# Kernel optimization log

Hardware: AMD Instinct MI355X
Metric: run time of the kernel (lower is better)

## Reference

```python
import jax, jax.numpy as jnp
import numpy as np

N1 = 50000        # nodes in g1
N_LAYERS = 3
N2 = N1 * N_LAYERS  # nodes in g2 (kron tiling)
E1 = 800000
E2 = 2400000
D = 64
LEAKY_SLOPE = 0.01


def graph_conv(x, src, dst, num_nodes, W, b):
    """DGL GraphConv with norm='both', in_feats == out_feats (aggregate-then-matmul).
    h = D_in^{-1/2} A D_out^{-1/2} x W + b, degrees clamped to >=1.
    """
    ones_e = jnp.ones(src.shape[0], dtype=x.dtype)
    out_deg = jax.ops.segment_sum(ones_e, src, num_segments=num_nodes)
    in_deg = jax.ops.segment_sum(ones_e, dst, num_segments=num_nodes)
    norm_src = jnp.power(jnp.clip(out_deg, 1.0), -0.5)  # [N]
    norm_dst = jnp.power(jnp.clip(in_deg, 1.0), -0.5)   # [N]
    feat = x * norm_src[:, None]                         # [N, D]
    agg = jax.ops.segment_sum(feat[src], dst, num_segments=num_nodes)  # [N, D]
    rst = agg * norm_dst[:, None]
    return rst @ W + b


def setup_inputs() -> dict:
    key = jax.random.key(0)
    k = jax.random.split(key, 8)
    return {
        "node_features": jax.random.normal(k[0], (N1, D), dtype=jnp.float32),
        "WQ": jax.random.normal(k[1], (D, D), dtype=jnp.float32) * (1.0 / np.sqrt(D)),
        "bQ": jnp.zeros((D,), dtype=jnp.float32),
        "WM": jax.random.normal(k[2], (D, D), dtype=jnp.float32) * (1.0 / np.sqrt(D)),
        "bM": jnp.zeros((D,), dtype=jnp.float32),
        "src1": jax.random.randint(k[3], (E1,), 0, N1, dtype=jnp.int32),
        "dst1": jax.random.randint(k[4], (E1,), 0, N1, dtype=jnp.int32),
        "src2": jax.random.randint(k[5], (E2,), 0, N2, dtype=jnp.int32),
        "dst2": jax.random.randint(k[6], (E2,), 0, N2, dtype=jnp.int32),
    }


def reference(node_features, WQ, bQ, WM, bM, src1, dst1, src2, dst2):
    h_Q1 = graph_conv(node_features, src1, dst1, N1, WQ, bQ)
    h_Q1 = jax.nn.leaky_relu(h_Q1, negative_slope=LEAKY_SLOPE)
    # torch.kron(ones(n_layers,1), h_Q1) == vertical tiling
    M_feat = jnp.tile(h_Q1, (N_LAYERS, 1))  # [N_LAYERS*N1, D]
    h_M1 = graph_conv(M_feat, src2, dst2, N2, WM, bM)
    return jax.nn.leaky_relu(h_M1, negative_slope=LEAKY_SLOPE)
```

## Files before the change

kernel.cpp:

```cpp
#include <hip/hip_runtime.h>
#include <hip/hip_fp16.h>

constexpr int cN1 = 50000;
constexpr int cN2 = 150000;
constexpr int cE1 = 800000;
constexpr int cE2 = 2400000;
constexpr int cD  = 64;
constexpr int MAXB = 640;
#define LEAKY 0.01f

constexpr int NB1 = (cN1 + 255) / 256;
constexpr int NB2 = (cN2 + 255) / 256;

constexpr int BD1 = 64, BD2 = 192, BS1 = 64, BS2 = 192, CVB = 256;
constexpr int PR0 = BD1;
constexpr int PR1 = PR0 + BD2;
constexpr int PR2 = PR1 + BS1;
constexpr int PR3 = PR2 + BS2;
constexpr int PR4 = PR3 + CVB;

constexpr int SD1 = 128, SD2 = 384, SS1 = 64, SS2 = 192;

__device__ __forceinline__ void bucket_count_region(
    const int* __restrict__ idx, int E4, int* __restrict__ bcnt, int nbuck,
    int b, int B, int* h) {
    for (int i = threadIdx.x; i < nbuck; i += 256) h[i] = 0;
    __syncthreads();
    const int4* v4 = (const int4*)idx;
    for (int i = b * 256 + threadIdx.x; i < E4; i += B * 256) {
        int4 v = v4[i];
        atomicAdd(&h[v.x >> 8], 1);
        atomicAdd(&h[v.y >> 8], 1);
        atomicAdd(&h[v.z >> 8], 1);
        atomicAdd(&h[v.w >> 8], 1);
    }
    __syncthreads();
    for (int i = threadIdx.x; i < nbuck; i += 256) {
        int c = h[i];
        if (c) atomicAdd(&bcnt[i], c);
    }
}

__global__ __launch_bounds__(256) void prep_kernel(
    const int* __restrict__ dst1, const int* __restrict__ dst2,
    const int* __restrict__ src1, const int* __restrict__ src2,
    const float* __restrict__ x, __half* __restrict__ xh,
    int* __restrict__ bcntD1, int* __restrict__ bcntD2,
    int* __restrict__ bcntS1, int* __restrict__ bcntS2) {
    __shared__ int h[MAXB];
    int b = blockIdx.x;
    if (b < PR0) {
        bucket_count_region(dst1, cE1 / 4, bcntD1, NB1, b, BD1, h);
    } else if (b < PR1) {
        bucket_count_region(dst2, cE2 / 4, bcntD2, NB2, b - PR0, BD2, h);
    } else if (b < PR2) {
        bucket_count_region(src1, cE1 / 4, bcntS1, NB1, b - PR1, BS1, h);
    } else if (b < PR3) {
        bucket_count_region(src2, cE2 / 4, bcntS2, NB2, b - PR2, BS2, h);
    } else {
        int i = (b - PR3) * 256 + threadIdx.x;
        const int n4 = cN1 * cD / 4;
        for (; i < n4; i += CVB * 256) {
            float4 v = ((const float4*)x)[i];
            __half2* o = (__half2*)xh;
            o[2 * i]     = __floats2half2_rn(v.x, v.y);
            o[2 * i + 1] = __floats2half2_rn(v.z, v.w);
        }
    }
}

__global__ __launch_bounds__(256) void scan4_kernel(
    int* __restrict__ bcntD1, int* __restrict__ bbaseD1, int* __restrict__ bcurD1,
    int* __restrict__ bcntD2, int* __restrict__ bbaseD2, int* __restrict__ bcurD2,
    int* __restrict__ bcntS1, int* __restrict__ bbaseS1, int* __restrict__ bcurS1,
    int* __restrict__ bcntS2, int* __restrict__ bbaseS2, int* __restrict__ bcurS2,
    int* __restrict__ offs1, int* __restrict__ offs2) {
    int b = blockIdx.x;
    int tid = threadIdx.x;
    int* bcnt; int* bbase; int* bcur; int n; int e;
    if (b == 0)      { bcnt = bcntD1; bbase = bbaseD1; bcur = bcurD1; n = NB1; e = cE1; }
    else if (b == 1) { bcnt = bcntD2; bbase = bbaseD2; bcur = bcurD2; n = NB2; e = cE2; }
    else if (b == 2) { bcnt = bcntS1; bbase = bbaseS1; bcur = bcurS1; n = NB1; e = cE1; }
    else             { bcnt = bcntS2; bbase = bbaseS2; bcur = bcurS2; n = NB2; e = cE2; }
    if (b == 0 && tid == 0) offs1[cN1] = cE1;
    if (b == 1 && tid == 0) offs2[cN2] = cE2;
    __shared__ int s[256];
    int v[4];
    int t = 0;
#pragma unroll
    for (int j = 0; j < 4; ++j) { int i = tid * 4 + j; v[j] = (i < n) ? bcnt[i] : 0; t += v[j]; }
    s[tid] = t; __syncthreads();
    for (int off = 1; off < 256; off <<= 1) {
        int a = (tid >= off) ? s[tid - off] : 0;
        __syncthreads();
        s[tid] += a;
        __syncthreads();
    }
    int run = s[tid] - t;
#pragma unroll
    for (int j = 0; j < 4; ++j) {
        int i = tid * 4 + j;
        if (i < n) { bbase[i] = run; bcur[i] = run; run += v[j]; }
    }
    if (tid == 0) bbase[n] = e;
}

__global__ __launch_bounds__(256) void scatter4_kernel(
    const int* __restrict__ src1, const int* __restrict__ dst1,
    int* __restrict__ bcurD1, unsigned int* __restrict__ pairs1,
    const int* __restrict__ src2, const int* __restrict__ dst2,
    int* __restrict__ bcurD2, unsigned int* __restrict__ pairs2,
    int* __restrict__ bcurS1, unsigned char* __restrict__ sval1,
    int* __restrict__ bcurS2, unsigned char* __restrict__ sval2) {
    __shared__ int hist[MAXB];
    __shared__ int cur[MAXB];
    int tid = threadIdx.x;
    int bx = blockIdx.x;
    bool pairMode;
    const int* key; const int* pay; int* bcur;
    unsigned int* pout = nullptr; unsigned char* bout = nullptr;
    int nbuck, E, blk, nblk;
    if (bx < SD1) {
        pairMode = true;  key = dst1; pay = src1; bcur = bcurD1; pout = pairs1;
        nbuck = NB1; E = cE1; blk = bx; nblk = SD1;
    } else if (bx < SD1 + SD2) {
        pairMode = true;  key = dst2; pay = src2; bcur = bcurD2; pout = pairs2;
        nbuck = NB2; E = cE2; blk = bx - SD1; nblk = SD2;
    } else if (bx < SD1 + SD2 + SS1) {
        pairMode = false; key = src1; pay = nullptr; bcur = bcurS1; bout = sval1;
        nbuck = NB1; E = cE1; blk = bx - SD1 - SD2; nblk = SS1;
    } else {
        pairMode = false; key = src2; pay = nullptr; bcur = bcurS2; bout = sval2;
        nbuck = NB2; E = cE2; blk = bx - SD1 - SD2 - SS1; nblk = SS2;
    }
    int spe = (((E / 4) + nblk - 1) / nblk) * 4;
    int b0 = blk * spe;
    int b1 = b0 + spe; if (b1 > E) b1 = E;
    for (int i = tid; i < nbuck; i += 256) hist[i] = 0;
    __syncthreads();
    for (int i = b0 + tid * 4; i < b1; i += 1024) {
        int4 d = *(const int4*)(key + i);
        atomicAdd(&hist[d.x >> 8], 1);
        atomicAdd(&hist[d.y >> 8], 1);
        atomicAdd(&hist[d.z >> 8], 1);
        atomicAdd(&hist[d.w >> 8], 1);
    }
    __syncthreads();
    for (int i = tid; i < nbuck; i += 256) cur[i] = atomicAdd(&bcur[i], hist[i]);
    __syncthreads();
    if (pairMode) {
        for (int i = b0 + tid * 4; i < b1; i += 1024) {
            int4 d = *(const int4*)(key + i);
            int4 s = *(const int4*)(pay + i);
            int p0 = atomicAdd(&cur[d.x >> 8], 1);
            pout[p0] = ((unsigned)(d.x & 255) << 24) | (unsigned)s.x;
            int p1 = atomicAdd(&cur[d.y >> 8], 1);
            pout[p1] = ((unsigned)(d.y & 255) << 24) | (unsigned)s.y;
            int p2 = atomicAdd(&cur[d.z >> 8], 1);
            pout[p2] = ((unsigned)(d.z & 255) << 24) | (unsigned)s.z;
            int p3 = atomicAdd(&cur[d.w >> 8], 1);
            pout[p3] = ((unsigned)(d.w & 255) << 24) | (unsigned)s.w;
        }
    } else {
        for (int i = b0 + tid * 4; i < b1; i += 1024) {
            int4 d = *(const int4*)(key + i);
            int p0 = atomicAdd(&cur[d.x >> 8], 1); bout[p0] = (unsigned char)(d.x & 255);
            int p1 = atomicAdd(&cur[d.y >> 8], 1); bout[p1] = (unsigned char)(d.y & 255);
            int p2 = atomicAdd(&cur[d.z >> 8], 1); bout[p2] = (unsigned char)(d.z & 255);
            int p3 = atomicAdd(&cur[d.w >> 8], 1); bout[p3] = (unsigned char)(d.w & 255);
        }
    }
}

__global__ __launch_bounds__(256) void sbin_kernel(
    const unsigned char* __restrict__ sval1, const int* __restrict__ bbaseS1,
    float* __restrict__ nsrc1,
    const unsigned char* __restrict__ sval2, const int* __restrict__ bbaseS2,
    float* __restrict__ nsrc2) {
    const unsigned char* sv; const int* bbase; float* nsrc; int N, bk;
    if (blockIdx.x < NB1) { sv = sval1; bbase = bbaseS1; nsrc = nsrc1; N = cN1; bk = blockIdx.x; }
    else                  { sv = sval2; bbase = bbaseS2; nsrc = nsrc2; N = cN2; bk = blockIdx.x - NB1; }
    __shared__ int cnt[256];
    int tid = threadIdx.x;
    cnt[tid] = 0;
    __syncthreads();
    int k0 = bbase[bk];
    int k1 = bbase[bk + 1];
    for (int k = k0 + tid; k < k1; k += 256) atomicAdd(&cnt[sv[k]], 1);
    __syncthreads();
    int lo = bk << 8;
    int span = N - lo; if (span > 256) span = 256;
    if (tid < span) {
        int d = cnt[tid];
        d = d < 1 ? 1 : d;
        nsrc[lo + tid] = rsqrtf((float)d);
    }
}

__global__ __launch_bounds__(256) void bin12_kernel(
    const unsigned int* __restrict__ pairs1, const int* __restrict__ bbase1,
    const float* __restrict__ nsrc1, unsigned int* __restrict__ sorted1,
    int* __restrict__ offs1,
    const unsigned int* __restrict__ pairs2, const int* __restrict__ bbase2,
    const float* __restrict__ nsrc2, unsigned int* __restrict__ sorted2,
    int* __restrict__ offs2) {
    const unsigned int* pairs; const int* bbase; const float* nsrc;
    unsigned int* sorted; int* offs; int N, foldn, bk;
    if (blockIdx.x < NB1) {
        pairs = pairs1; bbase = bbase1; nsrc = nsrc1; sorted = sorted1;
        offs = offs1; N = cN1; foldn = 0; bk = blockIdx.x;
    } else {
        pairs = pairs2; bbase = bbase2; nsrc = nsrc2; sorted = sorted2;
        offs = offs2; N = cN2; foldn = cN1; bk = blockIdx.x - NB1;
    }
    __shared__ int cnt[256];
    __shared__ int s[256];
    __shared__ int cur[256];
    int tid = threadIdx.x;
    int lo = bk << 8;
    int span = N - lo; if (span > 256) span = 256;
    int k0 = bbase[bk];
    int k1 = bbase[bk + 1];
    cnt[tid] = 0;
    __syncthreads();
    for (int k = k0 + tid; k < k1; k += 256) atomicAdd(&cnt[pairs[k] >> 24], 1);
    __syncthreads();
    int v = cnt[tid];
    s[tid] = v; __syncthreads();
    for (int off = 1; off < 256; off <<= 1) {
        int a = (tid >= off) ? s[tid - off] : 0;
        __syncthreads();
        s[tid] += a;
        __syncthreads();
    }
    int excl = s[tid] - v;
    cur[tid] = k0 + excl;
    if (tid < span) offs[lo + tid] = k0 + excl;
    __syncthreads();
    for (int k = k0 + tid; k < k1; k += 256) {
        unsigned pr = pairs[k];
        int d = pr >> 24;
        int sidx = (int)(pr & 0xFFFFFFu);
        int r = sidx;
        if (foldn) {
            if (r >= 2 * foldn) r -= 2 * foldn;
            else if (r >= foldn) r -= foldn;
        }
        __half nh = __float2half(nsrc[sidx]);
        int pos = atomicAdd(&cur[d], 1);
        sorted[pos] = ((unsigned)__half_as_ushort(nh) << 16) | (unsigned)r;
    }
}

#define FMA8(v, nv)                                                     \
    {                                                                   \
        float2 f0 = __half22float2(*(const __half2*)&(v).x);            \
        float2 f1 = __half22float2(*(const __half2*)&(v).y);            \
        float2 f2 = __half22float2(*(const __half2*)&(v).z);            \
        float2 f3 = __half22float2(*(const __half2*)&(v).w);            \
        a0.x = fmaf(f0.x, nv, a0.x); a0.y = fmaf(f0.y, nv, a0.y);       \
        a0.z = fmaf(f1.x, nv, a0.z); a0.w = fmaf(f1.y, nv, a0.w);       \
        a1.x = fmaf(f2.x, nv, a1.x); a1.y = fmaf(f2.y, nv, a1.y);       \
        a1.z = fmaf(f3.x, nv, a1.z); a1.w = fmaf(f3.y, nv, a1.w);       \
    }

template <bool EPI>
__global__ __launch_bounds__(256) void agg_csr_kernel(
    const __half* __restrict__ feat, const unsigned int* __restrict__ sorted,
    const int* __restrict__ offs, float* __restrict__ outp,
    const float* __restrict__ bias, int N) {
    int w = (blockIdx.x * blockDim.x + threadIdx.x) >> 4;
    if (w >= N) return;
    int l16  = threadIdx.x & 15;
    int slot = l16 >> 3;
    int c    = l16 & 7;

    int k0 = offs[w];
    int k1 = offs[w + 1];
    float4 a0 = {0.f, 0.f, 0.f, 0.f};
    float4 a1 = {0.f, 0.f, 0.f, 0.f};

    int k = k0 + slot;
    for (; k + 2 < k1; k += 4) {
        unsigned eA = sorted[k];
        unsigned eB = sorted[k + 2];
        float nA = __half2float(__ushort_as_half((unsigned short)(eA >> 16)));
        float nB = __half2float(__ushort_as_half((unsigned short)(eB >> 16)));
        int rA = (int)(eA & 0xFFFFu);
        int rB = (int)(eB & 0xFFFFu);
        uint4 vA = *(const uint4*)(feat + (size_t)rA * cD + c * 8);
        uint4 vB = *(const uint4*)(feat + (size_t)rB * cD + c * 8);
        FMA8(vA, nA);
        FMA8(vB, nB);
    }
    if (k < k1) {
        unsigned e = sorted[k];
        float nv = __half2float(__ushort_as_half((unsigned short)(e >> 16)));
        int r = (int)(e & 0xFFFFu);
        uint4 v = *(const uint4*)(feat + (size_t)r * cD + c * 8);
        FMA8(v, nv);
    }

    a0.x += __shfl_xor(a0.x, 8); a0.y += __shfl_xor(a0.y, 8);
    a0.z += __shfl_xor(a0.z, 8); a0.w += __shfl_xor(a0.w, 8);
    a1.x += __shfl_xor(a1.x, 8); a1.y += __shfl_xor(a1.y, 8);
    a1.z += __shfl_xor(a1.z, 8); a1.w += __shfl_xor(a1.w, 8);

    if (slot == 0) {
        if (EPI) {
            int dg = k1 - k0;
            float nd = rsqrtf((float)(dg < 1 ? 1 : dg));
            float4 b0 = *(const float4*)(bias + c * 8);
            float4 b1 = *(const float4*)(bias + c * 8 + 4);
            float4 r0, r1;
            r0.x = fmaf(a0.x, nd, b0.x); r0.y = fmaf(a0.y, nd, b0.y);
            r0.z = fmaf(a0.z, nd, b0.z); r0.w = fmaf(a0.w, nd, b0.w);
            r1.x = fmaf(a1.x, nd, b1.x); r1.y = fmaf(a1.y, nd, b1.y);
            r1.z = fmaf(a1.z, nd, b1.z); r1.w = fmaf(a1.w, nd, b1.w);
            r0.x = r0.x > 0.f ? r0.x : LEAKY * r0.x;
            r0.y = r0.y > 0.f ? r0.y : LEAKY * r0.y;
            r0.z = r0.z > 0.f ? r0.z : LEAKY * r0.z;
            r0.w = r0.w > 0.f ? r0.w : LEAKY * r0.w;
            r1.x = r1.x > 0.f ? r1.x : LEAKY * r1.x;
            r1.y = r1.y > 0.f ? r1.y : LEAKY * r1.y;
            r1.z = r1.z > 0.f ? r1.z : LEAKY * r1.z;
            r1.w = r1.w > 0.f ? r1.w : LEAKY * r1.w;
            *(float4*)(outp + (size_t)w * cD + c * 8) = r0;
            *(float4*)(outp + (size_t)w * cD + c * 8 + 4) = r1;
        } else {
            *(float4*)(outp + (size_t)w * cD + c * 8) = a0;
            *(float4*)(outp + (size_t)w * cD + c * 8 + 4) = a1;
        }
    }
}
#undef FMA8

constexpr int GR = 32;
constexpr int RP = 36;

__global__ __launch_bounds__(256) void gemm12_kernel(
    const float* __restrict__ A, const int* __restrict__ offs,
    const float* __restrict__ WQ_, const float* __restrict__ bQ_,
    const float* __restrict__ WM_, __half* __restrict__ g, int N) {
    __shared__ float W1s[64 * 64];
    __shared__ float W2s[64 * 64];
    __shared__ float Rs_t[64 * RP];
    __shared__ float Hs_t[64 * RP];
    __shared__ float rn_s[GR];
    int tid = threadIdx.x;
    int row0 = blockIdx.x * GR;

    for (int i = tid; i < 64 * 64; i += 256) {
        W1s[i] = WQ_[i];
        W2s[i] = WM_[i];
    }
    if (tid < GR) {
        int row = row0 + tid;
        if (row < N) {
            int dg = offs[row + 1] - offs[row];
            rn_s[tid] = rsqrtf((float)(dg < 1 ? 1 : dg));
        } else {
            rn_s[tid] = 0.f;
        }
    }
    __syncthreads();
    for (int i = tid; i < GR * 64; i += 256) {
        int r = i >> 6;
        int k = i & 63;
        int row = row0 + r;
        float v = (row < N) ? A[(size_t)row * cD + k] * rn_s[r] : 0.f;
        Rs_t[k * RP + r] = v;
    }
    __syncthreads();

    int j  = tid & 63;
    int gq = tid >> 6;
    int r0 = gq * 8;

    float acc[8];
    float bq = bQ_[j];
#pragma unroll
    for (int i = 0; i < 8; ++i) acc[i] = bq;
#pragma unroll 8
    for (int k = 0; k < 64; ++k) {
        float wv = W1s[k * 64 + j];
        float4 ra = *(const float4*)&Rs_t[k * RP + r0];
        float4 rb = *(const float4*)&Rs_t[k * RP + r0 + 4];
        acc[0] = fmaf(ra.x, wv, acc[0]); acc[1] = fmaf(ra.y, wv, acc[1]);
        acc[2] = fmaf(ra.z, wv, acc[2]); acc[3] = fmaf(ra.w, wv, acc[3]);
        acc[4] = fmaf(rb.x, wv, acc[4]); acc[5] = fmaf(rb.y, wv, acc[5]);
        acc[6] = fmaf(rb.z, wv, acc[6]); acc[7] = fmaf(rb.w, wv, acc[7]);
    }
    float4 h0, h1;
    h0.x = acc[0] > 0.f ? acc[0] : LEAKY * acc[0];
    h0.y = acc[1] > 0.f ? acc[1] : LEAKY * acc[1];
    h0.z = acc[2] > 0.f ? acc[2] : LEAKY * acc[2];
    h0.w = acc[3] > 0.f ? acc[3] : LEAKY * acc[3];
    h1.x = acc[4] > 0.f ? acc[4] : LEAKY * acc[4];
    h1.y = acc[5] > 0.f ? acc[5] : LEAKY * acc[5];
    h1.z = acc[6] > 0.f ? acc[6] : LEAKY * acc[6];
    h1.w = acc[7] > 0.f ? acc[7] : LEAKY * acc[7];
    *(float4*)&Hs_t[j * RP + r0]     = h0;
    *(float4*)&Hs_t[j * RP + r0 + 4] = h1;
    __syncthreads();

    float acc2[8];
#pragma unroll
    for (int i = 0; i < 8; ++i) acc2[i] = 0.f;
#pragma unroll 8
    for (int k = 0; k < 64; ++k) {
        float wv = W2s[k * 64 + j];
        float4 ra = *(const float4*)&Hs_t[k * RP + r0];
        float4 rb = *(const float4*)&Hs_t[k * RP + r0 + 4];
        acc2[0] = fmaf(ra.x, wv, acc2[0]); acc2[1] = fmaf(ra.y, wv, acc2[1]);
        acc2[2] = fmaf(ra.z, wv, acc2[2]); acc2[3] = fmaf(ra.w, wv, acc2[3]);
        acc2[4] = fmaf(rb.x, wv, acc2[4]); acc2[5] = fmaf(rb.y, wv, acc2[5]);
        acc2[6] = fmaf(rb.z, wv, acc2[6]); acc2[7] = fmaf(rb.w, wv, acc2[7]);
    }
#pragma unroll
    for (int i = 0; i < 8; ++i) {
        int row = row0 + r0 + i;
        if (row < N) g[(size_t)row * cD + j] = __float2half(acc2[i]);
    }
}

extern "C" void kernel_launch(void* const* d_in, const int* in_sizes, int n_in,
                              void* d_out, int out_size, void* d_ws, size_t ws_size,
                              hipStream_t stream) {
    const float* x    = (const float*)d_in[0];
    const float* WQ   = (const float*)d_in[1];
    const float* bQ   = (const float*)d_in[2];
    const float* WM   = (const float*)d_in[3];
    const float* bM   = (const float*)d_in[4];
    const int*   src1 = (const int*)d_in[5];
    const int*   dst1 = (const int*)d_in[6];
    const int*   src2 = (const int*)d_in[7];
    const int*   dst2 = (const int*)d_in[8];
    float* out = (float*)d_out;

    char* p = (char*)d_ws;
    int*    bcntD1 = (int*)p;    p += sizeof(int) * MAXB;
    int*    bcntD2 = (int*)p;    p += sizeof(int) * MAXB;
    int*    bcntS1 = (int*)p;    p += sizeof(int) * MAXB;
    int*    bcntS2 = (int*)p;    p += sizeof(int) * MAXB;
    int*    bbaseD1= (int*)p;    p += sizeof(int) * (MAXB + 1);
    int*    bbaseD2= (int*)p;    p += sizeof(int) * (MAXB + 1);
    int*    bbaseS1= (int*)p;    p += sizeof(int) * (MAXB + 1);
    int*    bbaseS2= (int*)p;    p += sizeof(int) * (MAXB + 1);
    int*    bcurD1 = (int*)p;    p += sizeof(int) * MAXB;
    int*    bcurD2 = (int*)p;    p += sizeof(int) * MAXB;
    int*    bcurS1 = (int*)p;    p += sizeof(int) * MAXB;
    int*    bcurS2 = (int*)p;    p += sizeof(int) * MAXB;
    float*  nsrc1  = (float*)p;  p += sizeof(float) * cN1;
    float*  nsrc2  = (float*)p;  p += sizeof(float) * cN2;
    int*    offs1  = (int*)p;    p += sizeof(int) * (cN1 + 1);
    int*    offs2  = (int*)p;    p += sizeof(int) * (cN2 + 1);
    unsigned int* sorted2 = (unsigned int*)p; p += sizeof(int) * cE2;
    __half* gh     = (__half*)p; p += sizeof(__half) * (size_t)cN1 * cD;

    int* dout_i = (int*)d_out;
    unsigned int*  pairs2  = (unsigned int*)dout_i;
    unsigned int*  pairs1  = (unsigned int*)(dout_i + cE2);
    __half*        xh      = (__half*)(dout_i + cE2 + cE1);
    float*         agg1buf = (float*)(dout_i + cE2 + cE1 + (size_t)cN1 * cD / 2);
    unsigned char* sval2   = (unsigned char*)(dout_i + 8000000);
    unsigned char* sval1   = (unsigned char*)(dout_i + 8600000);
    unsigned int*  sorted1 = (unsigned int*)(dout_i + ((size_t)cN2 * cD - cE1));

    hipMemsetAsync(bcntD1, 0, sizeof(int) * 4 * MAXB, stream);

    prep_kernel<<<PR4, 256, 0, stream>>>(dst1, dst2, src1, src2, x, xh,
                                         bcntD1, bcntD2, bcntS1, bcntS2);

    scan4_kernel<<<4, 256, 0, stream>>>(
        bcntD1, bbaseD1, bcurD1, bcntD2, bbaseD2, bcurD2,
        bcntS1, bbaseS1, bcurS1, bcntS2, bbaseS2, bcurS2, offs1, offs2);

    scatter4_kernel<<<SD1 + SD2 + SS1 + SS2, 256, 0, stream>>>(
        src1, dst1, bcurD1, pairs1, src2, dst2, bcurD2, pairs2,
        bcurS1, sval1, bcurS2, sval2);

    sbin_kernel<<<NB1 + NB2, 256, 0, stream>>>(
        sval1, bbaseS1, nsrc1, sval2, bbaseS2, nsrc2);

    bin12_kernel<<<NB1 + NB2, 256, 0, stream>>>(
        pairs1, bbaseD1, nsrc1, sorted1, offs1,
        pairs2, bbaseD2, nsrc2, sorted2, offs2);

    agg_csr_kernel<false><<<(cN1 + 15) / 16, 256, 0, stream>>>(
        xh, sorted1, offs1, agg1buf, nullptr, cN1);
    gemm12_kernel<<<(cN1 + GR - 1) / GR, 256, 0, stream>>>(
        agg1buf, offs1, WQ, bQ, WM, gh, cN1);

    agg_csr_kernel<true><<<(cN2 + 15) / 16, 256, 0, stream>>>(
        gh, sorted2, offs2, out, bM, cN2);
}
```

Measured before the change: 214.9 us.

## Widen sort buckets from 256 to 1024 nodes per coarse bin

The two-level counting sort now uses coarse buckets of 1024 nodes instead of 256. Packed pairs carry a 10-bit local destination and a 22-bit source, and the src-degree values are stored as 16-bit shorts. Fewer coarse buckets shrink the global scan and the shared histograms in the scatter kernel, and fewer, larger blocks run in the fine-binning kernels. In exchange each fine-binning block does more serial work with larger shared arrays, fewer blocks give less parallelism, and the scatter and sval writes carry more bytes. sorted1 also moves from the output buffer into the workspace, and the scatter grid sizes are retuned.

```diff
diff --git a/kernel.cpp b/kernel.cpp
--- a/kernel.cpp
+++ b/kernel.cpp
@@ -6,11 +6,14 @@
 constexpr int cE1 = 800000;
 constexpr int cE2 = 2400000;
 constexpr int cD  = 64;
-constexpr int MAXB = 640;
 #define LEAKY 0.01f
 
-constexpr int NB1 = (cN1 + 255) / 256;
-constexpr int NB2 = (cN2 + 255) / 256;
+constexpr int FB1 = (cN1 + 255) / 256;
+constexpr int FB2 = (cN2 + 255) / 256;
+constexpr int MAXFB = 640;
+constexpr int KB1 = (cN1 + 1023) / 1024;
+constexpr int KB2 = (cN2 + 1023) / 1024;
+constexpr int MAXKB = 160;
 
 constexpr int BD1 = 64, BD2 = 192, BS1 = 64, BS2 = 192, CVB = 256;
 constexpr int PR0 = BD1;
@@ -19,12 +22,12 @@
 constexpr int PR3 = PR2 + BS2;
 constexpr int PR4 = PR3 + CVB;
 
-constexpr int SD1 = 128, SD2 = 384, SS1 = 64, SS2 = 192;
+constexpr int SD1 = 128, SD2 = 256, SS1 = 32, SS2 = 96;
 
 __device__ __forceinline__ void bucket_count_region(
-    const int* __restrict__ idx, int E4, int* __restrict__ bcnt, int nbuck,
+    const int* __restrict__ idx, int E4, int* __restrict__ bcnt, int nbuckF,
     int b, int B, int* h) {
-    for (int i = threadIdx.x; i < nbuck; i += 256) h[i] = 0;
+    for (int i = threadIdx.x; i < nbuckF; i += 256) h[i] = 0;
     __syncthreads();
     const int4* v4 = (const int4*)idx;
     for (int i = b * 256 + threadIdx.x; i < E4; i += B * 256) {
@@ -35,9 +38,9 @@
         atomicAdd(&h[v.w >> 8], 1);
     }
     __syncthreads();
-    for (int i = threadIdx.x; i < nbuck; i += 256) {
+    for (int i = threadIdx.x; i < nbuckF; i += 256) {
         int c = h[i];
-        if (c) atomicAdd(&bcnt[i], c);
+        if (c) atomicAdd(&bcnt[i >> 2], c);
     }
 }
 
@@ -47,16 +50,16 @@
     const float* __restrict__ x, __half* __restrict__ xh,
     int* __restrict__ bcntD1, int* __restrict__ bcntD2,
     int* __restrict__ bcntS1, int* __restrict__ bcntS2) {
-    __shared__ int h[MAXB];
+    __shared__ int h[MAXFB];
     int b = blockIdx.x;
     if (b < PR0) {
-        bucket_count_region(dst1, cE1 / 4, bcntD1, NB1, b, BD1, h);
+        bucket_count_region(dst1, cE1 / 4, bcntD1, FB1, b, BD1, h);
     } else if (b < PR1) {
-        bucket_count_region(dst2, cE2 / 4, bcntD2, NB2, b - PR0, BD2, h);
+        bucket_count_region(dst2, cE2 / 4, bcntD2, FB2, b - PR0, BD2, h);
     } else if (b < PR2) {
-        bucket_count_region(src1, cE1 / 4, bcntS1, NB1, b - PR1, BS1, h);
+        bucket_count_region(src1, cE1 / 4, bcntS1, FB1, b - PR1, BS1, h);
     } else if (b < PR3) {
-        bucket_count_region(src2, cE2 / 4, bcntS2, NB2, b - PR2, BS2, h);
+        bucket_count_region(src2, cE2 / 4, bcntS2, FB2, b - PR2, BS2, h);
     } else {
         int i = (b - PR3) * 256 + threadIdx.x;
         const int n4 = cN1 * cD / 4;
@@ -78,30 +81,23 @@
     int b = blockIdx.x;
     int tid = threadIdx.x;
     int* bcnt; int* bbase; int* bcur; int n; int e;
-    if (b == 0)      { bcnt = bcntD1; bbase = bbaseD1; bcur = bcurD1; n = NB1; e = cE1; }
-    else if (b == 1) { bcnt = bcntD2; bbase = bbaseD2; bcur = bcurD2; n = NB2; e = cE2; }
-    else if (b == 2) { bcnt = bcntS1; bbase = bbaseS1; bcur = bcurS1; n = NB1; e = cE1; }
-    else             { bcnt = bcntS2; bbase = bbaseS2; bcur = bcurS2; n = NB2; e = cE2; }
+    if (b == 0)      { bcnt = bcntD1; bbase = bbaseD1; bcur = bcurD1; n = KB1; e = cE1; }
+    else if (b == 1) { bcnt = bcntD2; bbase = bbaseD2; bcur = bcurD2; n = KB2; e = cE2; }
+    else if (b == 2) { bcnt = bcntS1; bbase = bbaseS1; bcur = bcurS1; n = KB1; e = cE1; }
+    else             { bcnt = bcntS2; bbase = bbaseS2; bcur = bcurS2; n = KB2; e = cE2; }
     if (b == 0 && tid == 0) offs1[cN1] = cE1;
     if (b == 1 && tid == 0) offs2[cN2] = cE2;
     __shared__ int s[256];
-    int v[4];
-    int t = 0;
-#pragma unroll
-    for (int j = 0; j < 4; ++j) { int i = tid * 4 + j; v[j] = (i < n) ? bcnt[i] : 0; t += v[j]; }
-    s[tid] = t; __syncthreads();
+    int v = (tid < n) ? bcnt[tid] : 0;
+    s[tid] = v; __syncthreads();
     for (int off = 1; off < 256; off <<= 1) {
         int a = (tid >= off) ? s[tid - off] : 0;
         __syncthreads();
         s[tid] += a;
         __syncthreads();
     }
-    int run = s[tid] - t;
-#pragma unroll
-    for (int j = 0; j < 4; ++j) {
-        int i = tid * 4 + j;
-        if (i < n) { bbase[i] = run; bcur[i] = run; run += v[j]; }
-    }
+    int run = s[tid] - v;
+    if (tid < n) { bbase[tid] = run; bcur[tid] = run; }
     if (tid == 0) bbase[n] = e;
 }
 
@@ -110,28 +106,28 @@
     int* __restrict__ bcurD1, unsigned int* __restrict__ pairs1,
     const int* __restrict__ src2, const int* __restrict__ dst2,
     int* __restrict__ bcurD2, unsigned int* __restrict__ pairs2,
-    int* __restrict__ bcurS1, unsigned char* __restrict__ sval1,
-    int* __restrict__ bcurS2, unsigned char* __restrict__ sval2) {
-    __shared__ int hist[MAXB];
-    __shared__ int cur[MAXB];
+    int* __restrict__ bcurS1, unsigned short* __restrict__ sval1,
+    int* __restrict__ bcurS2, unsigned short* __restrict__ sval2) {
+    __shared__ int hist[MAXKB];
+    __shared__ int cur[MAXKB];
     int tid = threadIdx.x;
     int bx = blockIdx.x;
     bool pairMode;
     const int* key; const int* pay; int* bcur;
-    unsigned int* pout = nullptr; unsigned char* bout = nullptr;
+    unsigned int* pout = nullptr; unsigned short* sout = nullptr;
     int nbuck, E, blk, nblk;
     if (bx < SD1) {
         pairMode = true;  key = dst1; pay = src1; bcur = bcurD1; pout = pairs1;
-        nbuck = NB1; E = cE1; blk = bx; nblk = SD1;
+        nbuck = KB1; E = cE1; blk = bx; nblk = SD1;
     } else if (bx < SD1 + SD2) {
         pairMode = true;  key = dst2; pay = src2; bcur = bcurD2; pout = pairs2;
-        nbuck = NB2; E = cE2; blk = bx - SD1; nblk = SD2;
+        nbuck = KB2; E = cE2; blk = bx - SD1; nblk = SD2;
     } else if (bx < SD1 + SD2 + SS1) {
-        pairMode = false; key = src1; pay = nullptr; bcur = bcurS1; bout = sval1;
-        nbuck = NB1; E = cE1; blk = bx - SD1 - SD2; nblk = SS1;
+        pairMode = false; key = src1; pay = nullptr; bcur = bcurS1; sout = sval1;
+        nbuck = KB1; E = cE1; blk = bx - SD1 - SD2; nblk = SS1;
     } else {
-        pairMode = false; key = src2; pay = nullptr; bcur = bcurS2; bout = sval2;
-        nbuck = NB2; E = cE2; blk = bx - SD1 - SD2 - SS1; nblk = SS2;
+        pairMode = false; key = src2; pay = nullptr; bcur = bcurS2; sout = sval2;
+        nbuck = KB2; E = cE2; blk = bx - SD1 - SD2 - SS1; nblk = SS2;
     }
     int spe = (((E / 4) + nblk - 1) / nblk) * 4;
     int b0 = blk * spe;
@@ -140,10 +136,10 @@
     __syncthreads();
     for (int i = b0 + tid * 4; i < b1; i += 1024) {
         int4 d = *(const int4*)(key + i);
-        atomicAdd(&hist[d.x >> 8], 1);
-        atomicAdd(&hist[d.y >> 8], 1);
-        atomicAdd(&hist[d.z >> 8], 1);
-        atomicAdd(&hist[d.w >> 8], 1);
+        atomicAdd(&hist[d.x >> 10], 1);
+        atomicAdd(&hist[d.y >> 10], 1);
+        atomicAdd(&hist[d.z >> 10], 1);
+        atomicAdd(&hist[d.w >> 10], 1);
     }
     __syncthreads();
     for (int i = tid; i < nbuck; i += 256) cur[i] = atomicAdd(&bcur[i], hist[i]);
@@ -152,48 +148,48 @@
         for (int i = b0 + tid * 4; i < b1; i += 1024) {
             int4 d = *(const int4*)(key + i);
             int4 s = *(const int4*)(pay + i);
-            int p0 = atomicAdd(&cur[d.x >> 8], 1);
-            pout[p0] = ((unsigned)(d.x & 255) << 24) | (unsigned)s.x;
-            int p1 = atomicAdd(&cur[d.y >> 8], 1);
-            pout[p1] = ((unsigned)(d.y & 255) << 24) | (unsigned)s.y;
-            int p2 = atomicAdd(&cur[d.z >> 8], 1);
-            pout[p2] = ((unsigned)(d.z & 255) << 24) | (unsigned)s.z;
-            int p3 = atomicAdd(&cur[d.w >> 8], 1);
-            pout[p3] = ((unsigned)(d.w & 255) << 24) | (unsigned)s.w;
+            int p0 = atomicAdd(&cur[d.x >> 10], 1);
+            pout[p0] = ((unsigned)(d.x & 1023) << 22) | (unsigned)s.x;
+            int p1 = atomicAdd(&cur[d.y >> 10], 1);
+            pout[p1] = ((unsigned)(d.y & 1023) << 22) | (unsigned)s.y;
+            int p2 = atomicAdd(&cur[d.z >> 10], 1);
+            pout[p2] = ((unsigned)(d.z & 1023) << 22) | (unsigned)s.z;
+            int p3 = atomicAdd(&cur[d.w >> 10], 1);
+            pout[p3] = ((unsigned)(d.w & 1023) << 22) | (unsigned)s.w;
         }
     } else {
         for (int i = b0 + tid * 4; i < b1; i += 1024) {
             int4 d = *(const int4*)(key + i);
-            int p0 = atomicAdd(&cur[d.x >> 8], 1); bout[p0] = (unsigned char)(d.x & 255);
-            int p1 = atomicAdd(&cur[d.y >> 8], 1); bout[p1] = (unsigned char)(d.y & 255);
-            int p2 = atomicAdd(&cur[d.z >> 8], 1); bout[p2] = (unsigned char)(d.z & 255);
-            int p3 = atomicAdd(&cur[d.w >> 8], 1); bout[p3] = (unsigned char)(d.w & 255);
+            int p0 = atomicAdd(&cur[d.x >> 10], 1); sout[p0] = (unsigned short)(d.x & 1023);
+            int p1 = atomicAdd(&cur[d.y >> 10], 1); sout[p1] = (unsigned short)(d.y & 1023);
+            int p2 = atomicAdd(&cur[d.z >> 10], 1); sout[p2] = (unsigned short)(d.z & 1023);
+            int p3 = atomicAdd(&cur[d.w >> 10], 1); sout[p3] = (unsigned short)(d.w & 1023);
         }
     }
 }
 
 __global__ __launch_bounds__(256) void sbin_kernel(
-    const unsigned char* __restrict__ sval1, const int* __restrict__ bbaseS1,
+    const unsigned short* __restrict__ sval1, const int* __restrict__ bbaseS1,
     float* __restrict__ nsrc1,
-    const unsigned char* __restrict__ sval2, const int* __restrict__ bbaseS2,
+    const unsigned short* __restrict__ sval2, const int* __restrict__ bbaseS2,
     float* __restrict__ nsrc2) {
-    const unsigned char* sv; const int* bbase; float* nsrc; int N, bk;
-    if (blockIdx.x < NB1) { sv = sval1; bbase = bbaseS1; nsrc = nsrc1; N = cN1; bk = blockIdx.x; }
-    else                  { sv = sval2; bbase = bbaseS2; nsrc = nsrc2; N = cN2; bk = blockIdx.x - NB1; }
-    __shared__ int cnt[256];
+    const unsigned short* sv; const int* bbase; float* nsrc; int N, bk;
+    if (blockIdx.x < KB1) { sv = sval1; bbase = bbaseS1; nsrc = nsrc1; N = cN1; bk = blockIdx.x; }
+    else                  { sv = sval2; bbase = bbaseS2; nsrc = nsrc2; N = cN2; bk = blockIdx.x - KB1; }
+    __shared__ int cnt[1024];
     int tid = threadIdx.x;
-    cnt[tid] = 0;
+    for (int i = tid; i < 1024; i += 256) cnt[i] = 0;
     __syncthreads();
     int k0 = bbase[bk];
     int k1 = bbase[bk + 1];
     for (int k = k0 + tid; k < k1; k += 256) atomicAdd(&cnt[sv[k]], 1);
     __syncthreads();
-    int lo = bk << 8;
-    int span = N - lo; if (span > 256) span = 256;
-    if (tid < span) {
-        int d = cnt[tid];
+    int lo = bk << 10;
+    int span = N - lo; if (span > 1024) span = 1024;
+    for (int i = tid; i < span; i += 256) {
+        int d = cnt[i];
         d = d < 1 ? 1 : d;
-        nsrc[lo + tid] = rsqrtf((float)d);
+        nsrc[lo + i] = rsqrtf((float)d);
     }
 }
 
@@ -206,41 +202,49 @@
     int* __restrict__ offs2) {
     const unsigned int* pairs; const int* bbase; const float* nsrc;
     unsigned int* sorted; int* offs; int N, foldn, bk;
-    if (blockIdx.x < NB1) {
+    if (blockIdx.x < KB1) {
         pairs = pairs1; bbase = bbase1; nsrc = nsrc1; sorted = sorted1;
         offs = offs1; N = cN1; foldn = 0; bk = blockIdx.x;
     } else {
         pairs = pairs2; bbase = bbase2; nsrc = nsrc2; sorted = sorted2;
-        offs = offs2; N = cN2; foldn = cN1; bk = blockIdx.x - NB1;
-    }
-    __shared__ int cnt[256];
+        offs = offs2; N = cN2; foldn = cN1; bk = blockIdx.x - KB1;
+    }
+    __shared__ int cnt[1024];
     __shared__ int s[256];
-    __shared__ int cur[256];
+    __shared__ int cur[1024];
     int tid = threadIdx.x;
-    int lo = bk << 8;
-    int span = N - lo; if (span > 256) span = 256;
+    int lo = bk << 10;
+    int span = N - lo; if (span > 1024) span = 1024;
     int k0 = bbase[bk];
     int k1 = bbase[bk + 1];
-    cnt[tid] = 0;
-    __syncthreads();
-    for (int k = k0 + tid; k < k1; k += 256) atomicAdd(&cnt[pairs[k] >> 24], 1);
-    __syncthreads();
-    int v = cnt[tid];
-    s[tid] = v; __syncthreads();
+    for (int i = tid; i < 1024; i += 256) cnt[i] = 0;
+    __syncthreads();
+    for (int k = k0 + tid; k < k1; k += 256) atomicAdd(&cnt[pairs[k] >> 22], 1);
+    __syncthreads();
+    int v[4];
+    int t = 0;
+#pragma unroll
+    for (int j = 0; j < 4; ++j) { v[j] = cnt[tid * 4 + j]; t += v[j]; }
+    s[tid] = t; __syncthreads();
     for (int off = 1; off < 256; off <<= 1) {
         int a = (tid >= off) ? s[tid - off] : 0;
         __syncthreads();
         s[tid] += a;
         __syncthreads();
     }
-    int excl = s[tid] - v;
-    cur[tid] = k0 + excl;
-    if (tid < span) offs[lo + tid] = k0 + excl;
+    int run = k0 + s[tid] - t;
+#pragma unroll
+    for (int j = 0; j < 4; ++j) {
+        int idx = tid * 4 + j;
+        cur[idx] = run;
+        if (idx < span) offs[lo + idx] = run;
+        run += v[j];
+    }
     __syncthreads();
     for (int k = k0 + tid; k < k1; k += 256) {
         unsigned pr = pairs[k];
-        int d = pr >> 24;
-        int sidx = (int)(pr & 0xFFFFFFu);
+        int d = pr >> 22;
+        int sidx = (int)(pr & 0x3FFFFFu);
         int r = sidx;
         if (foldn) {
             if (r >= 2 * foldn) r -= 2 * foldn;
@@ -439,35 +443,35 @@
     float* out = (float*)d_out;
 
     char* p = (char*)d_ws;
-    int*    bcntD1 = (int*)p;    p += sizeof(int) * MAXB;
-    int*    bcntD2 = (int*)p;    p += sizeof(int) * MAXB;
-    int*    bcntS1 = (int*)p;    p += sizeof(int) * MAXB;
-    int*    bcntS2 = (int*)p;    p += sizeof(int) * MAXB;
-    int*    bbaseD1= (int*)p;    p += sizeof(int) * (MAXB + 1);
-    int*    bbaseD2= (int*)p;    p += sizeof(int) * (MAXB + 1);
-    int*    bbaseS1= (int*)p;    p += sizeof(int) * (MAXB + 1);
-    int*    bbaseS2= (int*)p;    p += sizeof(int) * (MAXB + 1);
-    int*    bcurD1 = (int*)p;    p += sizeof(int) * MAXB;
-    int*    bcurD2 = (int*)p;    p += sizeof(int) * MAXB;
-    int*    bcurS1 = (int*)p;    p += sizeof(int) * MAXB;
-    int*    bcurS2 = (int*)p;    p += sizeof(int) * MAXB;
+    int*    bcntD1 = (int*)p;    p += sizeof(int) * MAXKB;
+    int*    bcntD2 = (int*)p;    p += sizeof(int) * MAXKB;
+    int*    bcntS1 = (int*)p;    p += sizeof(int) * MAXKB;
+    int*    bcntS2 = (int*)p;    p += sizeof(int) * MAXKB;
+    int*    bbaseD1= (int*)p;    p += sizeof(int) * (MAXKB + 1);
+    int*    bbaseD2= (int*)p;    p += sizeof(int) * (MAXKB + 1);
+    int*    bbaseS1= (int*)p;    p += sizeof(int) * (MAXKB + 1);
+    int*    bbaseS2= (int*)p;    p += sizeof(int) * (MAXKB + 1);
+    int*    bcurD1 = (int*)p;    p += sizeof(int) * MAXKB;
+    int*    bcurD2 = (int*)p;    p += sizeof(int) * MAXKB;
+    int*    bcurS1 = (int*)p;    p += sizeof(int) * MAXKB;
+    int*    bcurS2 = (int*)p;    p += sizeof(int) * MAXKB;
     float*  nsrc1  = (float*)p;  p += sizeof(float) * cN1;
     float*  nsrc2  = (float*)p;  p += sizeof(float) * cN2;
     int*    offs1  = (int*)p;    p += sizeof(int) * (cN1 + 1);
     int*    offs2  = (int*)p;    p += sizeof(int) * (cN2 + 1);
     unsigned int* sorted2 = (unsigned int*)p; p += sizeof(int) * cE2;
+    unsigned int* sorted1 = (unsigned int*)p; p += sizeof(int) * cE1;
     __half* gh     = (__half*)p; p += sizeof(__half) * (size_t)cN1 * cD;
 
     int* dout_i = (int*)d_out;
-    unsigned int*  pairs2  = (unsigned int*)dout_i;
-    unsigned int*  pairs1  = (unsigned int*)(dout_i + cE2);
-    __half*        xh      = (__half*)(dout_i + cE2 + cE1);
-    float*         agg1buf = (float*)(dout_i + cE2 + cE1 + (size_t)cN1 * cD / 2);
-    unsigned char* sval2   = (unsigned char*)(dout_i + 8000000);
-    unsigned char* sval1   = (unsigned char*)(dout_i + 8600000);
-    unsigned int*  sorted1 = (unsigned int*)(dout_i + ((size_t)cN2 * cD - cE1));
-
-    hipMemsetAsync(bcntD1, 0, sizeof(int) * 4 * MAXB, stream);
+    unsigned int*   pairs2  = (unsigned int*)dout_i;
+    unsigned int*   pairs1  = (unsigned int*)(dout_i + cE2);
+    __half*         xh      = (__half*)(dout_i + cE2 + cE1);
+    float*          agg1buf = (float*)(dout_i + cE2 + cE1 + (size_t)cN1 * cD / 2);
+    unsigned short* sval1   = (unsigned short*)(dout_i + 8000000);
+    unsigned short* sval2   = (unsigned short*)(dout_i + 8400000);
+
+    hipMemsetAsync(bcntD1, 0, sizeof(int) * 4 * MAXKB, stream);
 
     prep_kernel<<<PR4, 256, 0, stream>>>(dst1, dst2, src1, src2, x, xh,
                                          bcntD1, bcntD2, bcntS1, bcntS2);
@@ -480,10 +484,10 @@
         src1, dst1, bcurD1, pairs1, src2, dst2, bcurD2, pairs2,
         bcurS1, sval1, bcurS2, sval2);
 
-    sbin_kernel<<<NB1 + NB2, 256, 0, stream>>>(
+    sbin_kernel<<<KB1 + KB2, 256, 0, stream>>>(
         sval1, bbaseS1, nsrc1, sval2, bbaseS2, nsrc2);
 
-    bin12_kernel<<<NB1 + NB2, 256, 0, stream>>>(
+    bin12_kernel<<<KB1 + KB2, 256, 0, stream>>>(
         pairs1, bbaseD1, nsrc1, sorted1, offs1,
         pairs2, bbaseD2, nsrc2, sorted2, offs2);
 
```

After: 494.1 us. 2.3x slower.
